# Kernel optimization log

Hardware: AMD Instinct MI355X
Metric: run time of the kernel (lower is better)

Reference implementation:

```python
import jax, jax.numpy as jnp
import numpy as np
from jax import lax

EPS = 1e-5
SLOPE = 0.1
BETA = 0.25


def lrelu(x):
    return jnp.where(x >= 0, x, SLOPE * x)


def bn(x, g, b):
    # training-mode BatchNorm2d: batch stats over (N, H, W), biased variance
    m = x.mean((0, 2, 3), keepdims=True)
    v = x.var((0, 2, 3), keepdims=True)
    return g[None, :, None, None] * (x - m) * lax.rsqrt(v + EPS) + b[None, :, None, None]


def conv2d(x, w, b, stride=1, pad=1):
    y = lax.conv_general_dilated(x, w, (stride, stride), [(pad, pad), (pad, pad)],
                                 dimension_numbers=('NCHW', 'OIHW', 'NCHW'))
    return y + b[None, :, None, None]


def conv_transpose2d(x, w, b):
    # torch ConvTranspose2d(k=3, stride=2, padding=1, output_padding=1): out = 2*in
    # implemented as conv of stride-dilated input with spatially-flipped, IO-swapped kernel
    wt = jnp.flip(w, (2, 3)).transpose(1, 0, 2, 3)  # (in,out,kh,kw) -> (out,in,kh,kw)
    y = lax.conv_general_dilated(x, wt, (1, 1), [(1, 2), (1, 2)], lhs_dilation=(2, 2),
                                 dimension_numbers=('NCHW', 'OIHW', 'NCHW'))
    return y + b[None, :, None, None]


def vqvae_forward(x, cb, e1_w, e1_b, bn1_g, bn1_b, e2_w, e2_b, bn2_g, bn2_b,
                  preq_w, preq_b, postq_w, postq_b,
                  d1_w, d1_b, bn3_g, bn3_b, d2_w, d2_b, bn4_g, bn4_b, d3_w, d3_b):
    # encoder
    h = lrelu(bn(conv2d(x, e1_w, e1_b, stride=2), bn1_g, bn1_b))
    h = lrelu(bn(conv2d(h, e2_w, e2_b, stride=2), bn2_g, bn2_b))
    pq = conv2d(h, preq_w, preq_b)  # (B, cb_dim, H, W)
    B, C, H, W = pq.shape
    z = pq.transpose(0, 2, 3, 1).reshape(-1, C)  # (B*H*W, C)
    # squared euclidean distances (argmin equals cdist argmin)
    d2 = ((z * z).sum(-1, keepdims=True) - 2.0 * z @ cb.T + (cb * cb).sum(-1)[None, :])
    idx = jnp.argmin(d2, axis=-1)  # (B*H*W,)
    q = cb[idx]  # gather, (B*H*W, C)
    codebook_loss = jnp.mean((lax.stop_gradient(z) - q) ** 2)
    commitment_loss = jnp.mean((lax.stop_gradient(q) - z) ** 2)
    quantized_loss = codebook_loss + BETA * commitment_loss
    q_st = z + lax.stop_gradient(q - z)  # straight-through
    zq = q_st.reshape(B, H, W, C).transpose(0, 3, 1, 2)
    # decoder
    h = conv2d(zq, postq_w, postq_b)
    h = lrelu(bn(conv_transpose2d(h, d1_w, d1_b), bn3_g, bn3_b))
    h = lrelu(bn(conv_transpose2d(h, d2_w, d2_b), bn4_g, bn4_b))
    out = jnp.tanh(conv2d(h, d3_w, d3_b))
    return out, quantized_loss


def setup_inputs() -> dict:
    key = jax.random.key(0)
    ks = jax.random.split(key, 16)
    f32 = jnp.float32
    K, D, CC = 1024, 64, 3

    def w(k, shape, fan_in):
        return (jax.random.normal(k, shape, f32) / np.sqrt(fan_in)).astype(f32)

    inp = {
        'x': jax.random.normal(ks[0], (16, CC, 256, 256), f32),
        'cb': jax.random.normal(ks[1], (K, D), f32),
        'e1_w': w(ks[2], (16, CC, 3, 3), CC * 9), 'e1_b': jnp.zeros((16,), f32),
        'bn1_g': jnp.ones((16,), f32), 'bn1_b': jnp.zeros((16,), f32),
        'e2_w': w(ks[3], (4, 16, 3, 3), 16 * 9), 'e2_b': jnp.zeros((4,), f32),
        'bn2_g': jnp.ones((4,), f32), 'bn2_b': jnp.zeros((4,), f32),
        'preq_w': w(ks[4], (D, 4, 3, 3), 4 * 9), 'preq_b': jnp.zeros((D,), f32),
        'postq_w': w(ks[5], (4, D, 3, 3), D * 9), 'postq_b': jnp.zeros((4,), f32),
        'd1_w': w(ks[6], (4, 16, 3, 3), 4 * 9), 'd1_b': jnp.zeros((16,), f32),  # (in,out,kh,kw)
        'bn3_g': jnp.ones((16,), f32), 'bn3_b': jnp.zeros((16,), f32),
        'd2_w': w(ks[7], (16, 32, 3, 3), 16 * 9), 'd2_b': jnp.zeros((32,), f32),
        'bn4_g': jnp.ones((32,), f32), 'bn4_b': jnp.zeros((32,), f32),
        'd3_w': w(ks[8], (CC, 32, 3, 3), 32 * 9), 'd3_b': jnp.zeros((CC,), f32),
    }
    return inp


def reference(x, cb, e1_w, e1_b, bn1_g, bn1_b, e2_w, e2_b, bn2_g, bn2_b,
              preq_w, preq_b, postq_w, postq_b,
              d1_w, d1_b, bn3_g, bn3_b, d2_w, d2_b, bn4_g, bn4_b, d3_w, d3_b):
    return vqvae_forward(x, cb, e1_w, e1_b, bn1_g, bn1_b, e2_w, e2_b, bn2_g, bn2_b,
                         preq_w, preq_b, postq_w, postq_b,
                         d1_w, d1_b, bn3_g, bn3_b, d2_w, d2_b, bn4_g, bn4_b, d3_w, d3_b)
```

## Files before the change

kernel.cpp:

```cpp
#include <hip/hip_runtime.h>
#include <math.h>

#define EPSV 1e-5
#define SLOPE 0.1f

typedef __attribute__((ext_vector_type(4))) float f32x4;
typedef __attribute__((ext_vector_type(8))) short short8x;

__device__ __forceinline__ float lrelu(float x){ return x >= 0.f ? x : SLOPE * x; }
__device__ __forceinline__ float tanh_fast(float x){
  float e = __expf(2.f * x);
  return 1.f - 2.f / (e + 1.f);
}
__device__ __forceinline__ unsigned bf16rne(float f){
  unsigned u = __float_as_uint(f);
  u += 0x7fff + ((u >> 16) & 1);
  return u >> 16;
}

template<int CL>
__device__ __forceinline__ void stats_epilogue(const float* sums, const float* sqs,
    double* __restrict__ part, int chbase, int P, int p, float* sred){
  const int C2 = 2 * CL;
  int t = threadIdx.x;
  #pragma unroll
  for (int c = 0; c < CL; c++){
    sred[t * C2 + c] = sums[c];
    sred[t * C2 + CL + c] = sqs[c];
  }
  __syncthreads();
  if (t < 64){
    int c = t % C2;
    int g = t / C2;
    const int G = 64 / C2;
    const int R = 256 / G;
    double s = 0;
    for (int r = g * R; r < (g + 1) * R; r++) s += (double)sred[r * C2 + c];
    #pragma unroll
    for (int off = C2; off < 64; off <<= 1) s += __shfl_xor(s, off);
    if (t < C2){
      int ch = chbase + (c < CL ? c : c - CL);
      part[(size_t)ch * 2 * P + (c < CL ? 0 : P) + p] = s;
    }
  }
}

__global__ __launch_bounds__(256) void bn_red_fin(const double* __restrict__ part, int P,
    const float* __restrict__ g, const float* __restrict__ b, float* __restrict__ ss, int C, double count){
  int c = blockIdx.x;
  __shared__ double r0[256], r1[256];
  int t = threadIdx.x;
  double s = 0, q = 0;
  for (int p = t; p < P; p += 256){
    s += part[(size_t)c * 2 * P + p];
    q += part[(size_t)c * 2 * P + P + p];
  }
  r0[t] = s; r1[t] = q; __syncthreads();
  for (int o = 128; o > 0; o >>= 1){
    if (t < o){ r0[t] += r0[t + o]; r1[t] += r1[t + o]; }
    __syncthreads();
  }
  if (t == 0){
    double m = r0[0] / count;
    double var = r1[0] / count - m * m;
    double scale = (double)g[c] / sqrt(var + EPSV);
    ss[c] = (float)scale;
    ss[C + c] = (float)((double)b[c] - m * scale);
  }
}

__global__ __launch_bounds__(256) void e1_conv(const float* __restrict__ x, const float* __restrict__ w,
    const float* __restrict__ bias, float* __restrict__ out, double* __restrict__ part){
  int idx = blockIdx.x * 256 + threadIdx.x;
  int ox2 = idx & 63, oy = (idx >> 6) & 127;
  int cog = (idx >> 13) & 1, n = idx >> 14;
  cog = __builtin_amdgcn_readfirstlane(cog);
  n   = __builtin_amdgcn_readfirstlane(n);
  float acc[8][2];
  #pragma unroll
  for (int co = 0; co < 8; co++){ float b = bias[cog * 8 + co]; acc[co][0] = b; acc[co][1] = b; }
  int ix0 = 4 * ox2 - 1;
  int lclamp = (ox2 > 0) ? ix0 : 0;
  const float* xp = x + (size_t)n * 3 * 65536;
  #pragma unroll
  for (int ci = 0; ci < 3; ci++){
    const float* pl = xp + ci * 65536;
    #pragma unroll
    for (int ky = 0; ky < 3; ky++){
      int iy = 2 * oy - 1 + ky;
      if (iy >= 0){
        const float* row = pl + iy * 256;
        float l = row[lclamp];
        float4 m = *(const float4*)(row + ix0 + 1);
        float v0 = (ox2 > 0) ? l : 0.f;
        #pragma unroll
        for (int co = 0; co < 8; co++){
          const float* wp = w + (((cog * 8 + co) * 3 + ci) * 3 + ky) * 3;
          acc[co][0] = fmaf(v0,  wp[0], acc[co][0]);
          acc[co][0] = fmaf(m.x, wp[1], acc[co][0]);
          acc[co][0] = fmaf(m.y, wp[2], acc[co][0]);
          acc[co][1] = fmaf(m.y, wp[0], acc[co][1]);
          acc[co][1] = fmaf(m.z, wp[1], acc[co][1]);
          acc[co][1] = fmaf(m.w, wp[2], acc[co][1]);
        }
      }
    }
  }
  float sums[8], sqs[8];
  #pragma unroll
  for (int co = 0; co < 8; co++){
    float2 st; st.x = acc[co][0]; st.y = acc[co][1];
    *(float2*)(out + ((size_t)(n * 16 + cog * 8 + co) * 128 + oy) * 128 + 2 * ox2) = st;
    sums[co] = acc[co][0] + acc[co][1];
    sqs[co] = acc[co][0] * acc[co][0] + acc[co][1] * acc[co][1];
  }
  __shared__ float sred[256 * 16];
  int p = ((blockIdx.x >> 6) << 5) + (blockIdx.x & 31);
  stats_epilogue<8>(sums, sqs, part, cog * 8, 512, p, sred);
}

__global__ __launch_bounds__(256) void e2_conv(const float* __restrict__ in, const float* __restrict__ w,
    const float* __restrict__ bias, const float* __restrict__ ssIn, float* __restrict__ out,
    double* __restrict__ part){
  int idx = blockIdx.x * 256 + threadIdx.x;
  int ox = idx & 63, oy = (idx >> 6) & 63, n = idx >> 12;
  float acc[4];
  #pragma unroll
  for (int j = 0; j < 4; j++) acc[j] = bias[j];
  int iy0 = oy * 2 - 1, ix0 = ox * 2 - 1;
  const float* ip = in + (size_t)n * 16 * 16384;
  #pragma unroll
  for (int ky = 0; ky < 3; ky++){
    int iy = iy0 + ky; if ((unsigned)iy >= 128u) continue;
    #pragma unroll
    for (int kx = 0; kx < 3; kx++){
      int ix = ix0 + kx; if ((unsigned)ix >= 128u) continue;
      const float* r = ip + iy * 128 + ix;
      #pragma unroll
      for (int ci = 0; ci < 16; ci++){
        float v = lrelu(fmaf(r[ci * 16384], ssIn[ci], ssIn[16 + ci]));
        #pragma unroll
        for (int co = 0; co < 4; co++)
          acc[co] = fmaf(v, w[(co * 16 + ci) * 9 + ky * 3 + kx], acc[co]);
      }
    }
  }
  float sums[4], sqs[4];
  #pragma unroll
  for (int co = 0; co < 4; co++){
    out[(((size_t)n * 4 + co) * 64 + oy) * 64 + ox] = acc[co];
    sums[co] = acc[co];
    sqs[co] = acc[co] * acc[co];
  }
  __shared__ float sred[256 * 8];
  stats_epilogue<4>(sums, sqs, part, 0, 256, blockIdx.x, sred);
}

__global__ __launch_bounds__(256) void preq_conv(const float* __restrict__ in, const float* __restrict__ w,
    const float* __restrict__ bias, const float* __restrict__ ssIn, float* __restrict__ Zq){
  int idx = blockIdx.x * 256 + threadIdx.x;
  int sp = idx & 65535;
  int coq = idx >> 16;
  int x = sp & 63, y = (sp >> 6) & 63, n = sp >> 12;
  float scv[4] = {ssIn[0], ssIn[1], ssIn[2], ssIn[3]};
  float shv[4] = {ssIn[4], ssIn[5], ssIn[6], ssIn[7]};
  float a0 = bias[coq * 4 + 0], a1 = bias[coq * 4 + 1], a2 = bias[coq * 4 + 2], a3 = bias[coq * 4 + 3];
  const float* ip = in + (size_t)n * 4 * 4096;
  #pragma unroll
  for (int ky = 0; ky < 3; ky++){
    int iy = y - 1 + ky; if ((unsigned)iy >= 64u) continue;
    #pragma unroll
    for (int kx = 0; kx < 3; kx++){
      int ix = x - 1 + kx; if ((unsigned)ix >= 64u) continue;
      #pragma unroll
      for (int ci = 0; ci < 4; ci++){
        float v = lrelu(fmaf(ip[ci * 4096 + iy * 64 + ix], scv[ci], shv[ci]));
        const float* wp = w + ((coq * 4) * 4 + ci) * 9 + ky * 3 + kx;
        a0 = fmaf(v, wp[0], a0);
        a1 = fmaf(v, wp[36], a1);
        a2 = fmaf(v, wp[72], a2);
        a3 = fmaf(v, wp[108], a3);
      }
    }
  }
  float4 o; o.x = a0; o.y = a1; o.z = a2; o.w = a3;
  ((float4*)Zq)[coq * 65536 + sp] = o;
}

__global__ __launch_bounds__(256) void prep_all(const float* __restrict__ cb, double* __restrict__ cb64,
    double* __restrict__ cbn64, float* __restrict__ cbn32, unsigned short* __restrict__ cbh,
    unsigned short* __restrict__ cbl, int* __restrict__ flagcnt,
    const float* __restrict__ pw, float* __restrict__ P){
  int t = threadIdx.x;
  if (blockIdx.x < 4){
    int k = blockIdx.x * 256 + t;
    if (k == 0) flagcnt[0] = 0;
    double s = 0;
    for (int d = 0; d < 64; d++){
      float v = cb[k * 64 + d];
      cb64[(size_t)k * 64 + d] = (double)v;
      s = fma((double)v, (double)v, s);
      unsigned h = bf16rne(v);
      float hf = __uint_as_float(h << 16);
      unsigned l = bf16rne(v - hf);
      cbh[k * 64 + d] = (unsigned short)h;
      cbl[k * 64 + d] = (unsigned short)l;
    }
    cbn64[k] = s;
    cbn32[k] = (float)s;
  } else {
    int gid = (blockIdx.x - 4) * 256 + t;
    if (gid >= 9216) return;
    int k = gid / 9, tap = gid - k * 9;
    float a0 = 0.f, a1 = 0.f, a2 = 0.f, a3 = 0.f;
    const float* cp = cb + (k << 6);
    #pragma unroll 16
    for (int ci = 0; ci < 64; ci++){
      float c = cp[ci];
      a0 = fmaf(c, pw[(0 * 64 + ci) * 9 + tap], a0);
      a1 = fmaf(c, pw[(1 * 64 + ci) * 9 + tap], a1);
      a2 = fmaf(c, pw[(2 * 64 + ci) * 9 + tap], a2);
      a3 = fmaf(c, pw[(3 * 64 + ci) * 9 + tap], a3);
    }
    float4 o; o.x = a0; o.y = a1; o.z = a2; o.w = a3;
    ((float4*)P)[gid] = o;
  }
}

__global__ __launch_bounds__(256) void vq_screen_mfma(const float* __restrict__ Zq,
    const unsigned short* __restrict__ cbh, const unsigned short* __restrict__ cbl,
    const float* __restrict__ cbn32, int* __restrict__ idxout,
    int* __restrict__ flagcnt, int* __restrict__ flaglist, float* __restrict__ stepb){
  __shared__ unsigned short lcb[32 * 64 * 8];
  __shared__ float lcn[128];
  int t = threadIdx.x;
  int lane = t & 63;
  int w = t >> 6;
  int col = lane & 15, hg = lane >> 4;
  int pos0 = blockIdx.x * 128 + w * 32;
  int posA = pos0 + col, posB = pos0 + 16 + col;
  const float4* Zq4 = (const float4*)Zq;
  short8x zhA[2], zlA[2], zhB[2], zlB[2];
  #pragma unroll
  for (int kc = 0; kc < 2; kc++){
    #pragma unroll
    for (int tb = 0; tb < 2; tb++){
      int pos = tb ? posB : posA;
      float4 f0 = Zq4[(size_t)(8 * kc + 2 * hg) * 65536 + pos];
      float4 f1 = Zq4[(size_t)(8 * kc + 2 * hg + 1) * 65536 + pos];
      float zv[8] = {f0.x, f0.y, f0.z, f0.w, f1.x, f1.y, f1.z, f1.w};
      union { unsigned u[4]; short8x v; } H, L;
      #pragma unroll
      for (int j = 0; j < 4; j++){
        unsigned h0 = bf16rne(zv[2 * j]);
        unsigned h1 = bf16rne(zv[2 * j + 1]);
        float hf0 = __uint_as_float(h0 << 16);
        float hf1 = __uint_as_float(h1 << 16);
        unsigned l0 = bf16rne(zv[2 * j] - hf0);
        unsigned l1 = bf16rne(zv[2 * j + 1] - hf1);
        H.u[j] = h0 | (h1 << 16);
        L.u[j] = l0 | (l1 << 16);
      }
      if (tb){ zhB[kc] = H.v; zlB[kc] = L.v; } else { zhA[kc] = H.v; zlA[kc] = L.v; }
    }
  }
  float BA = 3.0e38f, SA = 3.0e38f, BB = 3.0e38f, SBt = 3.0e38f;
  int IA = 0, IB = 0;
  for (int step = 0; step < 8; step++){
    int code0 = step * 128;
    __syncthreads();
    #pragma unroll
    for (int i = 0; i < 8; i++){
      int piece = i * 256 + t;
      int fb = piece >> 6, pl = piece & 63;
      int g = fb >> 2, kc = (fb >> 1) & 1, sp = fb & 1;
      const unsigned short* src = (sp ? cbl : cbh)
          + ((size_t)(code0 + g * 16 + (pl & 15)) << 6) + kc * 32 + ((pl >> 4) << 3);
      *(uint4*)&lcb[piece * 8] = *(const uint4*)src;
    }
    if (t < 128) lcn[t] = cbn32[code0 + t];
    __syncthreads();
    float bA = 3.0e38f, sA = 3.0e38f, bB = 3.0e38f, sB = 3.0e38f;
    int iA = 0, iB = 0;
    #pragma unroll 2
    for (int g = 0; g < 8; g++){
      const short8x* lc8 = (const short8x*)lcb;
      short8x Ah0 = lc8[(g * 4 + 0) * 64 + lane];
      short8x Al0 = lc8[(g * 4 + 1) * 64 + lane];
      short8x Ah1 = lc8[(g * 4 + 2) * 64 + lane];
      short8x Al1 = lc8[(g * 4 + 3) * 64 + lane];
      f32x4 accA = {0.f, 0.f, 0.f, 0.f};
      f32x4 accB = {0.f, 0.f, 0.f, 0.f};
      accA = __builtin_amdgcn_mfma_f32_16x16x32_bf16(Ah0, zhA[0], accA, 0, 0, 0);
      accA = __builtin_amdgcn_mfma_f32_16x16x32_bf16(Ah1, zhA[1], accA, 0, 0, 0);
      accA = __builtin_amdgcn_mfma_f32_16x16x32_bf16(Ah0, zlA[0], accA, 0, 0, 0);
      accA = __builtin_amdgcn_mfma_f32_16x16x32_bf16(Ah1, zlA[1], accA, 0, 0, 0);
      accA = __builtin_amdgcn_mfma_f32_16x16x32_bf16(Al0, zhA[0], accA, 0, 0, 0);
      accA = __builtin_amdgcn_mfma_f32_16x16x32_bf16(Al1, zhA[1], accA, 0, 0, 0);
      accB = __builtin_amdgcn_mfma_f32_16x16x32_bf16(Ah0, zhB[0], accB, 0, 0, 0);
      accB = __builtin_amdgcn_mfma_f32_16x16x32_bf16(Ah1, zhB[1], accB, 0, 0, 0);
      accB = __builtin_amdgcn_mfma_f32_16x16x32_bf16(Ah0, zlB[0], accB, 0, 0, 0);
      accB = __builtin_amdgcn_mfma_f32_16x16x32_bf16(Ah1, zlB[1], accB, 0, 0, 0);
      accB = __builtin_amdgcn_mfma_f32_16x16x32_bf16(Al0, zhB[0], accB, 0, 0, 0);
      accB = __builtin_amdgcn_mfma_f32_16x16x32_bf16(Al1, zhB[1], accB, 0, 0, 0);
      int cbase = code0 + g * 16 + 4 * hg;
      #pragma unroll
      for (int r = 0; r < 4; r++){
        float cn = lcn[g * 16 + 4 * hg + r];
        float vA = fmaf(accA[r], -2.0f, cn);
        sA = fminf(sA, fmaxf(vA, bA));
        if (vA < bA){ bA = vA; iA = cbase + r; }
        float vB = fmaf(accB[r], -2.0f, cn);
        sB = fminf(sB, fmaxf(vB, bB));
        if (vB < bB){ bB = vB; iB = cbase + r; }
      }
    }
    #pragma unroll
    for (int off = 16; off <= 32; off <<= 1){
      float ob = __shfl_xor(bA, off);
      float os = __shfl_xor(sA, off);
      int oi = __shfl_xor(iA, off);
      sA = fminf(fminf(sA, os), fmaxf(bA, ob));
      if (ob < bA){ bA = ob; iA = oi; }
      ob = __shfl_xor(bB, off);
      os = __shfl_xor(sB, off);
      oi = __shfl_xor(iB, off);
      sB = fminf(fminf(sB, os), fmaxf(bB, ob));
      if (ob < bB){ bB = ob; iB = oi; }
    }
    if (hg == 0){
      stepb[step * 65536 + posA] = bA;
      stepb[step * 65536 + posB] = bB;
    }
    if (bA < BA){ SA = fminf(BA, sA); BA = bA; IA = iA; } else SA = fminf(SA, bA);
    if (bB < BB){ SBt = fminf(BB, sB); BB = bB; IB = iB; } else SBt = fminf(SBt, bB);
  }
  if (hg == 0){
    idxout[posA] = IA;
    if (SA - BA < 1.2e-2f){
      int slot = atomicAdd(flagcnt, 1);
      flaglist[slot] = posA;
    }
    idxout[posB] = IB;
    if (SBt - BB < 1.2e-2f){
      int slot = atomicAdd(flagcnt, 1);
      flaglist[slot] = posB;
    }
  }
}

__global__ __launch_bounds__(256) void vq_refine(const float* __restrict__ Zq, const double* __restrict__ cb64,
    const double* __restrict__ cbn64, const int* __restrict__ flagcnt, const int* __restrict__ flaglist,
    const float* __restrict__ stepb, int* __restrict__ idxout){
  int gw = (blockIdx.x * 256 + threadIdx.x) >> 6;
  int lane = threadIdx.x & 63;
  int nf = flagcnt[0];
  for (int f = gw; f < nf; f += 512){
    int pos = flaglist[f];
    float zr[64];
    #pragma unroll
    for (int q = 0; q < 16; q++){
      float4 v = ((const float4*)Zq)[q * 65536 + pos];
      zr[4 * q] = v.x; zr[4 * q + 1] = v.y; zr[4 * q + 2] = v.z; zr[4 * q + 3] = v.w;
    }
    float sb[8];
    float B = 3.0e38f;
    #pragma unroll
    for (int s = 0; s < 8; s++){ sb[s] = stepb[s * 65536 + pos]; B = fminf(B, sb[s]); }
    float lim = B + 1.2e-2f;
    double best = 1e300; int bi = 1 << 30;
    #pragma unroll
    for (int s = 0; s < 8; s++){
      if (sb[s] < lim){
        int k0 = s * 128 + 2 * lane;
        #pragma unroll
        for (int kk = 0; kk < 2; kk++){
          int k = k0 + kk;
          const double* c = cb64 + (size_t)k * 64;
          double a0 = 0, a1 = 0, a2 = 0, a3 = 0;
          #pragma unroll
          for (int d = 0; d < 64; d += 4){
            a0 = fma(c[d], (double)zr[d], a0);
            a1 = fma(c[d + 1], (double)zr[d + 1], a1);
            a2 = fma(c[d + 2], (double)zr[d + 2], a2);
            a3 = fma(c[d + 3], (double)zr[d + 3], a3);
          }
          double sc = cbn64[k] - 2.0 * ((a0 + a1) + (a2 + a3));
          if (sc < best){ best = sc; bi = k; }
        }
      }
    }
    #pragma unroll
    for (int o = 32; o > 0; o >>= 1){
      double ob = __shfl_xor(best, o);
      int oi = __shfl_xor(bi, o);
      if (ob < best || (ob == best && oi < bi)){ best = ob; bi = oi; }
    }
    if (lane == 0) idxout[pos] = bi;
  }
}

__global__ __launch_bounds__(256) void postq_gather(const float* __restrict__ P, const int* __restrict__ idxm,
    const float* __restrict__ bias, float* __restrict__ out,
    const float* __restrict__ Zq, const float* __restrict__ cb, double* __restrict__ losspart){
  int gid = blockIdx.x * 256 + threadIdx.x;
  int sp = gid & 65535;
  int co = gid >> 16;
  co = __builtin_amdgcn_readfirstlane(co);
  int xx = sp & 63, yy = (sp >> 6) & 63, n = sp >> 12;
  float acc = bias[co];
  #pragma unroll
  for (int ky = 0; ky < 3; ky++){
    int iy = yy - 1 + ky; if ((unsigned)iy >= 64u) continue;
    #pragma unroll
    for (int kx = 0; kx < 3; kx++){
      int ix = xx - 1 + kx; if ((unsigned)ix >= 64u) continue;
      int spt = (n << 12) + (iy << 6) + ix;
      int k = idxm[spt];
      acc += P[(k * 9 + (ky * 3 + kx)) * 4 + co];
    }
  }
  out[((size_t)(n * 4 + co) << 12) + (yy << 6) + xx] = acc;
  if (co == 0){
    int k = idxm[sp];
    const float4* c4 = (const float4*)(cb + (k << 6));
    double l = 0;
    #pragma unroll
    for (int q = 0; q < 16; q++){
      float4 z = ((const float4*)Zq)[q * 65536 + sp];
      float4 c = c4[q];
      float d0 = z.x - c.x, d1 = z.y - c.y, d2 = z.z - c.z, d3 = z.w - c.w;
      l += (double)d0 * d0 + (double)d1 * d1 + (double)d2 * d2 + (double)d3 * d3;
    }
    __shared__ double sb[256];
    int t = threadIdx.x;
    sb[t] = l; __syncthreads();
    for (int o = 128; o > 0; o >>= 1){
      if (t < o) sb[t] += sb[t + o];
      __syncthreads();
    }
    if (t == 0) losspart[blockIdx.x] = sb[0];
  }
}

template<int CI, int CO, int IHt, int IWt, bool APPLY>
__global__ __launch_bounds__(256) void convT_cob8(const float* __restrict__ in, const float* __restrict__ w,
    const float* __restrict__ bias, const float* __restrict__ ssIn, float* __restrict__ out,
    double* __restrict__ part){
  constexpr int SB = IHt * IWt / 256;
  constexpr int COG = CO / 8;
  constexpr int P = 16 * SB;
  const int OW = IWt * 2;
  int idx = blockIdx.x * 256 + threadIdx.x;
  int ix = idx % IWt, iy = (idx / IWt) % IHt;
  int cog = (idx / (IWt * IHt)) % COG, n = idx / (IWt * IHt * COG);
  cog = __builtin_amdgcn_readfirstlane(cog);
  n   = __builtin_amdgcn_readfirstlane(n);
  float a00[8], a01[8], a10[8], a11[8];
  #pragma unroll
  for (int j = 0; j < 8; j++){ float b = bias[cog * 8 + j]; a00[j] = b; a01[j] = b; a10[j] = b; a11[j] = b; }
  bool okx = (ix + 1 < IWt), oky = (iy + 1 < IHt);
  int ixp = okx ? ix + 1 : ix, iyp = oky ? iy + 1 : iy;
  const float* ip = in + (size_t)n * CI * IHt * IWt;
  #pragma unroll 4
  for (int ci = 0; ci < CI; ci++){
    const float* p = ip + ci * IHt * IWt;
    float v00 = p[iy * IWt + ix];
    float v01 = p[iy * IWt + ixp];
    float v10 = p[iyp * IWt + ix];
    float v11 = p[iyp * IWt + ixp];
    if (APPLY){
      float sc = ssIn[ci], sh = ssIn[CI + ci];
      v00 = lrelu(fmaf(v00, sc, sh));
      v01 = lrelu(fmaf(v01, sc, sh));
      v10 = lrelu(fmaf(v10, sc, sh));
      v11 = lrelu(fmaf(v11, sc, sh));
    }
    if (!okx) v01 = 0.f;
    if (!oky) v10 = 0.f;
    if (!(okx && oky)) v11 = 0.f;
    const float* wp = w + ((size_t)ci * CO + cog * 8) * 9;
    #pragma unroll
    for (int j = 0; j < 8; j++){
      const float* q = wp + j * 9;
      a00[j] = fmaf(q[4], v00, a00[j]);
      a01[j] = fmaf(q[3], v01, a01[j]); a01[j] = fmaf(q[5], v00, a01[j]);
      a10[j] = fmaf(q[1], v10, a10[j]); a10[j] = fmaf(q[7], v00, a10[j]);
      a11[j] = fmaf(q[0], v11, a11[j]); a11[j] = fmaf(q[2], v10, a11[j]);
      a11[j] = fmaf(q[6], v01, a11[j]); a11[j] = fmaf(q[8], v00, a11[j]);
    }
  }
  float sums[8], sqs[8];
  #pragma unroll
  for (int j = 0; j < 8; j++){
    float* o = out + (((size_t)n * CO + cog * 8 + j) * (IHt * 2) + 2 * iy) * OW + 2 * ix;
    float2 r0; r0.x = a00[j]; r0.y = a01[j];
    float2 r1; r1.x = a10[j]; r1.y = a11[j];
    *(float2*)o = r0;
    *(float2*)(o + OW) = r1;
    sums[j] = (a00[j] + a01[j]) + (a10[j] + a11[j]);
    sqs[j] = (a00[j] * a00[j] + a01[j] * a01[j]) + (a10[j] * a10[j] + a11[j] * a11[j]);
  }
  __shared__ float sred[256 * 16];
  int sb = blockIdx.x % SB;
  stats_epilogue<8>(sums, sqs, part, cog * 8, P, n * SB + sb, sred);
}

__global__ __launch_bounds__(256) void d3_tile(const float* __restrict__ F, const float* __restrict__ w,
    const float* __restrict__ bias, const float* __restrict__ ss, float* __restrict__ out,
    const double* __restrict__ losspart){
  __shared__ float st[4 * 6 * 256];
  int t = threadIdx.x;
  int xg = t & 63, r = t >> 6;
  int n = blockIdx.x >> 6, oyb = blockIdx.x & 63;
  int oy = oyb * 4 + r;
  if (blockIdx.x == 0 && t < 64){
    double s = losspart[t] + losspart[t + 64] + losspart[t + 128] + losspart[t + 192];
    #pragma unroll
    for (int o = 32; o > 0; o >>= 1) s += __shfl_xor(s, o);
    if (t == 0) out[3145728] = (float)(1.25 * s / (65536.0 * 64.0));
  }
  float acc[3][4];
  #pragma unroll
  for (int co = 0; co < 3; co++){
    float b = bias[co];
    #pragma unroll
    for (int j = 0; j < 4; j++) acc[co][j] = b;
  }
  const float* base = F + (size_t)n * 32 * 65536;
  for (int cc = 0; cc < 8; cc++){
    int cib = cc * 4;
    #pragma unroll
    for (int j = 0; j < 6; j++){
      int p = j * 256 + t;
      int cl = p / 384, rem = p - cl * 384;
      int rr = rem >> 6, xq = rem & 63;
      int g = oyb * 4 - 1 + rr;
      float4 v;
      if ((unsigned)g < 256u){
        v = *(const float4*)(base + ((size_t)(cib + cl) * 256 + g) * 256 + 4 * xq);
        float sc = ss[cib + cl], sh = ss[32 + cib + cl];
        v.x = lrelu(fmaf(v.x, sc, sh));
        v.y = lrelu(fmaf(v.y, sc, sh));
        v.z = lrelu(fmaf(v.z, sc, sh));
        v.w = lrelu(fmaf(v.w, sc, sh));
      } else {
        v.x = 0.f; v.y = 0.f; v.z = 0.f; v.w = 0.f;
      }
      *(float4*)&st[((cl * 6 + rr) << 8) | (4 * xq)] = v;
    }
    __syncthreads();
    #pragma unroll
    for (int cl = 0; cl < 4; cl++){
      #pragma unroll
      for (int ky = 0; ky < 3; ky++){
        int rr = r + ky;
        float4 A = *(const float4*)&st[((cl * 6 + rr) << 8) | (4 * xg)];
        float Lv = __shfl_up(A.w, 1);
        float Rv = __shfl_down(A.x, 1);
        float u0 = (xg == 0) ? 0.f : Lv;
        float u5 = (xg == 63) ? 0.f : Rv;
        float u[6] = {u0, A.x, A.y, A.z, A.w, u5};
        #pragma unroll
        for (int co = 0; co < 3; co++){
          const float* wp = w + ((co * 32 + cib + cl) * 9) + ky * 3;
          #pragma unroll
          for (int j = 0; j < 4; j++){
            acc[co][j] = fmaf(u[j],     wp[0], acc[co][j]);
            acc[co][j] = fmaf(u[j + 1], wp[1], acc[co][j]);
            acc[co][j] = fmaf(u[j + 2], wp[2], acc[co][j]);
          }
        }
      }
    }
    __syncthreads();
  }
  #pragma unroll
  for (int co = 0; co < 3; co++){
    float4 s0;
    s0.x = tanh_fast(acc[co][0]); s0.y = tanh_fast(acc[co][1]);
    s0.z = tanh_fast(acc[co][2]); s0.w = tanh_fast(acc[co][3]);
    float* o = out + ((size_t)(n * 3 + co) * 256 + oy) * 256 + 4 * xg;
    *(float4*)o = s0;
  }
}

extern "C" void kernel_launch(void* const* d_in, const int* in_sizes, int n_in,
                              void* d_out, int out_size, void* d_ws, size_t ws_size,
                              hipStream_t stream){
  const float* x      = (const float*)d_in[0];
  const float* cb     = (const float*)d_in[1];
  const float* e1_w   = (const float*)d_in[2];
  const float* e1_b   = (const float*)d_in[3];
  const float* bn1_g  = (const float*)d_in[4];
  const float* bn1_b  = (const float*)d_in[5];
  const float* e2_w   = (const float*)d_in[6];
  const float* e2_b   = (const float*)d_in[7];
  const float* bn2_g  = (const float*)d_in[8];
  const float* bn2_b  = (const float*)d_in[9];
  const float* preq_w = (const float*)d_in[10];
  const float* preq_b = (const float*)d_in[11];
  const float* postq_w= (const float*)d_in[12];
  const float* postq_b= (const float*)d_in[13];
  const float* d1_w   = (const float*)d_in[14];
  const float* d1_b   = (const float*)d_in[15];
  const float* bn3_g  = (const float*)d_in[16];
  const float* bn3_b  = (const float*)d_in[17];
  const float* d2_w   = (const float*)d_in[18];
  const float* d2_b   = (const float*)d_in[19];
  const float* bn4_g  = (const float*)d_in[20];
  const float* bn4_b  = (const float*)d_in[21];
  const float* d3_w   = (const float*)d_in[22];
  const float* d3_b   = (const float*)d_in[23];
  float* out = (float*)d_out;
  char* ws = (char*)d_ws;

  double* losspart = (double*)ws;
  int*    flagcnt  = (int*)(ws + 2048);
  float*  ss       = (float*)(ws + 4096);
  double* cb64     = (double*)(ws + 8192);
  double* cbn64    = (double*)(ws + 532480);
  float*  cbn32    = (float*)(ws + 540672);
  unsigned short* cbh = (unsigned short*)(ws + 544768);
  unsigned short* cbl = (unsigned short*)(ws + 675840);
  int*    flaglist = (int*)(ws + 806912);
  int*    idx      = (int*)(ws + 1069056);
  double* part_e1  = (double*)(ws + 1331200);
  double* part_e2  = (double*)(ws + 1462272);
  float*  Ptab     = (float*)(ws + 1478656);
  double* part_d1  = (double*)(ws + 1478656);
  float*  A        = (float*)(ws + 2097152);
  float*  B        = (float*)(ws + 18874368);
  float*  Zq       = (float*)(ws + 19922944);
  double* part_d2  = (double*)(ws + 19922944);
  float*  F        = (float*)(ws + 36700160);
  float*  stepb    = (float*)(ws + 36700160);

  float *ss1 = ss + 0, *ss2 = ss + 32, *ss3 = ss + 48, *ss4 = ss + 80;
  float* D = B;

  prep_all<<<40, 256, 0, stream>>>(cb, cb64, cbn64, cbn32, cbh, cbl, flagcnt, postq_w, Ptab);

  e1_conv<<<1024, 256, 0, stream>>>(x, e1_w, e1_b, A, part_e1);
  bn_red_fin<<<16, 256, 0, stream>>>(part_e1, 512, bn1_g, bn1_b, ss1, 16, 262144.0);
  e2_conv<<<256, 256, 0, stream>>>(A, e2_w, e2_b, ss1, B, part_e2);
  bn_red_fin<<<4, 256, 0, stream>>>(part_e2, 256, bn2_g, bn2_b, ss2, 4, 65536.0);
  preq_conv<<<4096, 256, 0, stream>>>(B, preq_w, preq_b, ss2, Zq);

  vq_screen_mfma<<<512, 256, 0, stream>>>(Zq, cbh, cbl, cbn32, idx, flagcnt, flaglist, stepb);
  vq_refine<<<128, 256, 0, stream>>>(Zq, cb64, cbn64, flagcnt, flaglist, stepb, idx);

  postq_gather<<<1024, 256, 0, stream>>>(Ptab, idx, postq_b, D, Zq, cb, losspart);
  convT_cob8<4, 16, 64, 64, false><<<512, 256, 0, stream>>>(D, d1_w, d1_b, nullptr, A, part_d1);
  bn_red_fin<<<16, 256, 0, stream>>>(part_d1, 256, bn3_g, bn3_b, ss3, 16, 262144.0);
  convT_cob8<16, 32, 128, 128, true><<<4096, 256, 0, stream>>>(A, d2_w, d2_b, ss3, F, part_d2);
  bn_red_fin<<<32, 256, 0, stream>>>(part_d2, 1024, bn4_g, bn4_b, ss4, 32, 1048576.0);
  d3_tile<<<1024, 256, 0, stream>>>(F, d3_w, d3_b, ss4, out, losspart);
}
```

Baseline: 283.1 us.

## Pad stats LDS stride, split e2 by channel, halve d3 tiles along x

Pads the per-thread stats scratch stride to an odd count to avoid LDS bank conflicts in the BN partial-sum epilogue. e2_conv now computes one output channel per thread across four times as many blocks, with a double-precision tree reduction for BN stats. d3_tile uses 128-thread blocks covering half a row width, with a halo loaded into shared memory instead of wave shuffles. The goal is more parallelism and occupancy in small kernels, at the cost of redundant input reads in e2 and extra halo loads in d3.

```diff
diff --git a/kernel.cpp b/kernel.cpp
--- a/kernel.cpp
+++ b/kernel.cpp
@@ -22,11 +22,12 @@
 __device__ __forceinline__ void stats_epilogue(const float* sums, const float* sqs,
     double* __restrict__ part, int chbase, int P, int p, float* sred){
   const int C2 = 2 * CL;
+  const int ST = C2 + 1;
   int t = threadIdx.x;
   #pragma unroll
   for (int c = 0; c < CL; c++){
-    sred[t * C2 + c] = sums[c];
-    sred[t * C2 + CL + c] = sqs[c];
+    sred[t * ST + c] = sums[c];
+    sred[t * ST + CL + c] = sqs[c];
   }
   __syncthreads();
   if (t < 64){
@@ -35,7 +36,7 @@
     const int G = 64 / C2;
     const int R = 256 / G;
     double s = 0;
-    for (int r = g * R; r < (g + 1) * R; r++) s += (double)sred[r * C2 + c];
+    for (int r = g * R; r < (g + 1) * R; r++) s += (double)sred[r * ST + c];
     #pragma unroll
     for (int off = C2; off < 64; off <<= 1) s += __shfl_xor(s, off);
     if (t < C2){
@@ -114,7 +115,7 @@
     sums[co] = acc[co][0] + acc[co][1];
     sqs[co] = acc[co][0] * acc[co][0] + acc[co][1] * acc[co][1];
   }
-  __shared__ float sred[256 * 16];
+  __shared__ float sred[256 * 17];
   int p = ((blockIdx.x >> 6) << 5) + (blockIdx.x & 31);
   stats_epilogue<8>(sums, sqs, part, cog * 8, 512, p, sred);
 }
@@ -122,13 +123,15 @@
 __global__ __launch_bounds__(256) void e2_conv(const float* __restrict__ in, const float* __restrict__ w,
     const float* __restrict__ bias, const float* __restrict__ ssIn, float* __restrict__ out,
     double* __restrict__ part){
-  int idx = blockIdx.x * 256 + threadIdx.x;
-  int ox = idx & 63, oy = (idx >> 6) & 63, n = idx >> 12;
-  float acc[4];
-  #pragma unroll
-  for (int j = 0; j < 4; j++) acc[j] = bias[j];
+  int gid = blockIdx.x * 256 + threadIdx.x;
+  int sp = gid & 65535;
+  int co = gid >> 16;
+  co = __builtin_amdgcn_readfirstlane(co);
+  int ox = sp & 63, oy = (sp >> 6) & 63, n = sp >> 12;
+  float acc = bias[co];
   int iy0 = oy * 2 - 1, ix0 = ox * 2 - 1;
   const float* ip = in + (size_t)n * 16 * 16384;
+  const float* wb = w + co * 144;
   #pragma unroll
   for (int ky = 0; ky < 3; ky++){
     int iy = iy0 + ky; if ((unsigned)iy >= 128u) continue;
@@ -139,21 +142,25 @@
       #pragma unroll
       for (int ci = 0; ci < 16; ci++){
         float v = lrelu(fmaf(r[ci * 16384], ssIn[ci], ssIn[16 + ci]));
-        #pragma unroll
-        for (int co = 0; co < 4; co++)
-          acc[co] = fmaf(v, w[(co * 16 + ci) * 9 + ky * 3 + kx], acc[co]);
-      }
-    }
-  }
-  float sums[4], sqs[4];
-  #pragma unroll
-  for (int co = 0; co < 4; co++){
-    out[(((size_t)n * 4 + co) * 64 + oy) * 64 + ox] = acc[co];
-    sums[co] = acc[co];
-    sqs[co] = acc[co] * acc[co];
-  }
-  __shared__ float sred[256 * 8];
-  stats_epilogue<4>(sums, sqs, part, 0, 256, blockIdx.x, sred);
+        acc = fmaf(v, wb[ci * 9 + ky * 3 + kx], acc);
+      }
+    }
+  }
+  out[(((size_t)n * 4 + co) * 64 + oy) * 64 + ox] = acc;
+  __shared__ double s0[256], s1[256];
+  int t = threadIdx.x;
+  s0[t] = (double)acc;
+  s1[t] = (double)acc * (double)acc;
+  __syncthreads();
+  for (int o = 128; o > 0; o >>= 1){
+    if (t < o){ s0[t] += s0[t + o]; s1[t] += s1[t + o]; }
+    __syncthreads();
+  }
+  if (t == 0){
+    int p = blockIdx.x & 255;
+    part[(size_t)co * 512 + p] = s0[0];
+    part[(size_t)co * 512 + 256 + p] = s1[0];
+  }
 }
 
 __global__ __launch_bounds__(256) void preq_conv(const float* __restrict__ in, const float* __restrict__ w,
@@ -501,18 +508,18 @@
     sums[j] = (a00[j] + a01[j]) + (a10[j] + a11[j]);
     sqs[j] = (a00[j] * a00[j] + a01[j] * a01[j]) + (a10[j] * a10[j] + a11[j] * a11[j]);
   }
-  __shared__ float sred[256 * 16];
+  __shared__ float sred[256 * 17];
   int sb = blockIdx.x % SB;
   stats_epilogue<8>(sums, sqs, part, cog * 8, P, n * SB + sb, sred);
 }
 
-__global__ __launch_bounds__(256) void d3_tile(const float* __restrict__ F, const float* __restrict__ w,
+__global__ __launch_bounds__(128) void d3_tile(const float* __restrict__ F, const float* __restrict__ w,
     const float* __restrict__ bias, const float* __restrict__ ss, float* __restrict__ out,
     const double* __restrict__ losspart){
-  __shared__ float st[4 * 6 * 256];
+  __shared__ float st[4 * 6 * 136];
   int t = threadIdx.x;
-  int xg = t & 63, r = t >> 6;
-  int n = blockIdx.x >> 6, oyb = blockIdx.x & 63;
+  int xl = t & 31, r = t >> 5;
+  int n = blockIdx.x >> 7, oyb = (blockIdx.x >> 1) & 63, xh = blockIdx.x & 1;
   int oy = oyb * 4 + r;
   if (blockIdx.x == 0 && t < 64){
     double s = losspart[t] + losspart[t + 64] + losspart[t + 128] + losspart[t + 192];
@@ -528,38 +535,41 @@
     for (int j = 0; j < 4; j++) acc[co][j] = b;
   }
   const float* base = F + (size_t)n * 32 * 65536;
+  int gx0 = xh * 128 - 4;
   for (int cc = 0; cc < 8; cc++){
     int cib = cc * 4;
     #pragma unroll
-    for (int j = 0; j < 6; j++){
-      int p = j * 256 + t;
-      int cl = p / 384, rem = p - cl * 384;
-      int rr = rem >> 6, xq = rem & 63;
-      int g = oyb * 4 - 1 + rr;
-      float4 v;
-      if ((unsigned)g < 256u){
-        v = *(const float4*)(base + ((size_t)(cib + cl) * 256 + g) * 256 + 4 * xq);
-        float sc = ss[cib + cl], sh = ss[32 + cib + cl];
-        v.x = lrelu(fmaf(v.x, sc, sh));
-        v.y = lrelu(fmaf(v.y, sc, sh));
-        v.z = lrelu(fmaf(v.z, sc, sh));
-        v.w = lrelu(fmaf(v.w, sc, sh));
-      } else {
-        v.x = 0.f; v.y = 0.f; v.z = 0.f; v.w = 0.f;
-      }
-      *(float4*)&st[((cl * 6 + rr) << 8) | (4 * xq)] = v;
+    for (int j = 0; j < 7; j++){
+      int p = j * 128 + t;
+      if (p < 816){
+        int xq = p % 34;
+        int rem = p / 34;
+        int rr = rem % 6, cl = rem / 6;
+        int g = oyb * 4 - 1 + rr;
+        int gx = gx0 + 4 * xq;
+        float4 v;
+        if ((unsigned)g < 256u && (unsigned)gx <= 252u){
+          v = *(const float4*)(base + ((size_t)(cib + cl) * 256 + g) * 256 + gx);
+          float sc = ss[cib + cl], sh = ss[32 + cib + cl];
+          v.x = lrelu(fmaf(v.x, sc, sh));
+          v.y = lrelu(fmaf(v.y, sc, sh));
+          v.z = lrelu(fmaf(v.z, sc, sh));
+          v.w = lrelu(fmaf(v.w, sc, sh));
+        } else {
+          v.x = 0.f; v.y = 0.f; v.z = 0.f; v.w = 0.f;
+        }
+        *(float4*)&st[(cl * 6 + rr) * 136 + 4 * xq] = v;
+      }
     }
     __syncthreads();
     #pragma unroll
     for (int cl = 0; cl < 4; cl++){
       #pragma unroll
       for (int ky = 0; ky < 3; ky++){
-        int rr = r + ky;
-        float4 A = *(const float4*)&st[((cl * 6 + rr) << 8) | (4 * xg)];
-        float Lv = __shfl_up(A.w, 1);
-        float Rv = __shfl_down(A.x, 1);
-        float u0 = (xg == 0) ? 0.f : Lv;
-        float u5 = (xg == 63) ? 0.f : Rv;
+        int rowb = (cl * 6 + r + ky) * 136;
+        float4 A = *(const float4*)&st[rowb + 4 + 4 * xl];
+        float u0 = st[rowb + 3 + 4 * xl];
+        float u5 = st[rowb + 8 + 4 * xl];
         float u[6] = {u0, A.x, A.y, A.z, A.w, u5};
         #pragma unroll
         for (int co = 0; co < 3; co++){
@@ -580,7 +590,7 @@
     float4 s0;
     s0.x = tanh_fast(acc[co][0]); s0.y = tanh_fast(acc[co][1]);
     s0.z = tanh_fast(acc[co][2]); s0.w = tanh_fast(acc[co][3]);
-    float* o = out + ((size_t)(n * 3 + co) * 256 + oy) * 256 + 4 * xg;
+    float* o = out + ((size_t)(n * 3 + co) * 256 + oy) * 256 + xh * 128 + 4 * xl;
     *(float4*)o = s0;
   }
 }
@@ -643,7 +653,7 @@
 
   e1_conv<<<1024, 256, 0, stream>>>(x, e1_w, e1_b, A, part_e1);
   bn_red_fin<<<16, 256, 0, stream>>>(part_e1, 512, bn1_g, bn1_b, ss1, 16, 262144.0);
-  e2_conv<<<256, 256, 0, stream>>>(A, e2_w, e2_b, ss1, B, part_e2);
+  e2_conv<<<1024, 256, 0, stream>>>(A, e2_w, e2_b, ss1, B, part_e2);
   bn_red_fin<<<4, 256, 0, stream>>>(part_e2, 256, bn2_g, bn2_b, ss2, 4, 65536.0);
   preq_conv<<<4096, 256, 0, stream>>>(B, preq_w, preq_b, ss2, Zq);
 
@@ -655,5 +665,5 @@
   bn_red_fin<<<16, 256, 0, stream>>>(part_d1, 256, bn3_g, bn3_b, ss3, 16, 262144.0);
   convT_cob8<16, 32, 128, 128, true><<<4096, 256, 0, stream>>>(A, d2_w, d2_b, ss3, F, part_d2);
   bn_red_fin<<<32, 256, 0, stream>>>(part_d2, 1024, bn4_g, bn4_b, ss4, 32, 1048576.0);
-  d3_tile<<<1024, 256, 0, stream>>>(F, d3_w, d3_b, ss4, out, losspart);
-}
+  d3_tile<<<2048, 128, 0, stream>>>(F, d3_w, d3_b, ss4, out, losspart);
+}
```

Measured after the change: 285.3 us. About the same (+0.8%).
